# Performance work log

Hardware: AMD Instinct MI355X
Metric: run time of the kernel (lower is better)

Reference implementation:

```python
import jax, jax.numpy as jnp
import numpy as np

B, H, S, D = 1, 16, 2048, 64


def setup_inputs() -> dict:
    key = jax.random.key(0)
    kq, kk, kv, km = jax.random.split(key, 4)
    q = jax.random.normal(kq, (B, H, S, D), dtype=jnp.float32)
    k = jax.random.normal(kk, (B, H, S, D), dtype=jnp.float32)
    v = jax.random.normal(kv, (B, H, S, D), dtype=jnp.float32)
    omask = jax.random.uniform(km, (B, H, S, S), dtype=jnp.float32)
    return {"q": q, "k": k, "v": v, "omask": omask}


def reference(q, k, v, omask):
    # mask = omask / sqrt(rowsum(omask)), nan -> 0
    row_sum = jnp.sum(omask, axis=-1, keepdims=True)  # [B,H,S,1]
    decay_mask = jnp.nan_to_num(omask / jnp.sqrt(row_sum), nan=0.0)
    # retention = (q k^T) * mask  -> [B,H,S,S]
    retention = jnp.einsum("bhsd,bhtd->bhst", q, k) * decay_mask
    # normalize by |rowsum(retention)| clamped to >= 1 (detached in original)
    scale = jnp.clip(jnp.abs(jnp.sum(retention, axis=-1, keepdims=True)), 1.0, None)
    retention = retention / scale
    # output = retention @ v -> [B,H,S,D]
    return jnp.einsum("bhst,bhtd->bhsd", retention, v)
```

## Files before the change

### kernel.cpp

```cpp
#include <hip/hip_runtime.h>

#define H 16
#define S 2048
#define D 64
#define BM 64
#define BN 64
#define NT (S / BN)

typedef __attribute__((ext_vector_type(8))) short bf16x8;
typedef __attribute__((ext_vector_type(4))) short short4v;
typedef __attribute__((ext_vector_type(4))) float fx4;

static __device__ __forceinline__ short f2bf(float x) {
    unsigned u = __float_as_uint(x);
    u += 0x7fffu + ((u >> 16) & 1u);
    return (short)(u >> 16);
}
static __device__ __forceinline__ float bf2f(short s) {
    return __uint_as_float(((unsigned)(unsigned short)s) << 16);
}
static __device__ __forceinline__ void gl_lds16(const void* g, void* l) {
    __builtin_amdgcn_global_load_lds(
        (const __attribute__((address_space(1))) unsigned int*)g,
        (__attribute__((address_space(3))) unsigned int*)l, 16, 0, 0);
}

__global__ __launch_bounds__(256)
void ParallelRetention_prep_kernel(
    const float* __restrict__ k, const float* __restrict__ v,
    short* __restrict__ khi, short* __restrict__ klo, short* __restrict__ vt)
{
    __shared__ short lv[64 * 72];
    const int tid = threadIdx.x;
    const int h  = blockIdx.x & 15;
    const int sb = blockIdx.x >> 4;
    const int s0 = sb * 64;
    const int t_base = (tid >> 4) << 2;
    const int d4     = (tid & 15) << 2;
    const size_t hoff = (size_t)h * S * D;

    {
        const float* kb = k + hoff + (size_t)(s0 + t_base) * D + d4;
#pragma unroll
        for (int r = 0; r < 4; ++r) {
            fx4 kr = *(const fx4*)(kb + (size_t)r * D);
            short4v h4, l4;
#pragma unroll
            for (int j = 0; j < 4; ++j) {
                short hi = f2bf(kr[j]);
                h4[j] = hi;
                l4[j] = f2bf(kr[j] - bf2f(hi));
            }
            *(short4v*)(&khi[hoff + (size_t)(s0 + t_base + r) * D + d4]) = h4;
            *(short4v*)(&klo[hoff + (size_t)(s0 + t_base + r) * D + d4]) = l4;
        }
    }
    {
        const float* vb = v + hoff + (size_t)(s0 + t_base) * D + d4;
        fx4 vr[4];
#pragma unroll
        for (int r = 0; r < 4; ++r) vr[r] = *(const fx4*)(vb + (size_t)r * D);
#pragma unroll
        for (int j = 0; j < 4; ++j) {
            short4v p;
#pragma unroll
            for (int r = 0; r < 4; ++r) p[r] = f2bf(vr[r][j]);
            *(short4v*)(&lv[(d4 + j) * 72 + t_base]) = p;
        }
    }
    __syncthreads();
    {
        const int d = tid >> 2;
        const int c = tid & 3;
        bf16x8 a = *(const bf16x8*)(&lv[d * 72 + c * 16]);
        bf16x8 b = *(const bf16x8*)(&lv[d * 72 + c * 16 + 8]);
        short* o = vt + (size_t)h * D * S + (size_t)d * S + s0 + c * 16;
        *(bf16x8*)(o)     = a;
        *(bf16x8*)(o + 8) = b;
    }
}

__global__ __launch_bounds__(256, 2)
void ParallelRetention_origin_25374666785438_kernel(
    const float* __restrict__ q, const float* __restrict__ om,
    const short* __restrict__ khi, const short* __restrict__ klo,
    const short* __restrict__ vt, float* __restrict__ out)
{
    __shared__ short ldsKh[2][64 * 64];
    __shared__ short ldsKl[2][64 * 64];
    __shared__ short ldsVT[2][64 * 64];
    __shared__ short ldsP[64 * 64];

    const int tid  = threadIdx.x;
    const int wave = tid >> 6;
    const int lane = tid & 63;
    const int col  = lane & 15;
    const int quad = lane >> 4;

    const int h  = blockIdx.x & 15;
    const int qb = blockIdx.x >> 4;
    const int row0 = qb * BM;

    const size_t headQK = (size_t)h * S * D;
    const size_t headM  = (size_t)h * S * S;

    bf16x8 qh[2], qlo[2];
    {
        const int s_row = row0 + wave * 16 + col;
        const float* qp = q + headQK + (size_t)s_row * D + quad * 8;
#pragma unroll
        for (int c = 0; c < 2; ++c) {
            fx4 a = *(const fx4*)(qp + c * 32);
            fx4 b = *(const fx4*)(qp + c * 32 + 4);
            float f[8] = {a[0],a[1],a[2],a[3],b[0],b[1],b[2],b[3]};
#pragma unroll
            for (int j = 0; j < 8; ++j) {
                short hi = f2bf(f[j]);
                qh[c][j]  = hi;
                qlo[c][j] = f2bf(f[j] - bf2f(hi));
            }
        }
    }

    fx4 U[4];
#pragma unroll
    for (int nt = 0; nt < 4; ++nt) { U[nt][0]=0.f; U[nt][1]=0.f; U[nt][2]=0.f; U[nt][3]=0.f; }
    float rs_acc = 0.f, T_acc = 0.f;

    const int xq   = quad ^ (col & 3);
    const int cx   = (col >> 2) & 1;
    const int rdC0 = col * 64 + xq * 8 + cx * 32;
    const int rdC1 = col * 64 + xq * 8 + (cx ^ 1) * 32;
    const int prow   = wave * 16 + col;
    const int pwBase = prow * 64 + (quad & 1) * 4 + (((quad >> 1) ^ (col & 1))) * 8;
    const int pxor   = (col >> 1) & 3;
    const int prC0   = prow * 64 + xq * 8 + cx * 32;
    const int prC1   = prow * 64 + xq * 8 + (cx ^ 1) * 32;
    const int rowl = lane >> 3;
    const int swz8 = ((lane & 7) ^ rowl) * 8;
    const int kSrcOff = rowl * 64 + swz8;
    const int vSrcOff = rowl * 2048 + swz8;

    const short* khiH = khi + headQK;
    const short* kloH = klo + headQK;
    const short* vtH  = vt + (size_t)h * D * S;
    const float* omp0 = om + headM + (size_t)(row0 + wave * 16 + col) * S + quad * 4;

    auto stage = [&](int t0, short* dKh, short* dKl, short* dVT) {
        const short* ks = khiH + (size_t)t0 * 64 + kSrcOff;
        const short* ls = kloH + (size_t)t0 * 64 + kSrcOff;
        const short* vs = vtH + t0 + vSrcOff;
#pragma unroll
        for (int c = 0; c < 6; ++c) {
            int id = wave * 6 + c;
            int j  = id & 7;
            int tile = id >> 3;
            if (tile == 0)      gl_lds16(ks + j * 512, dKh + j * 512);
            else if (tile == 1) gl_lds16(ls + j * 512, dKl + j * 512);
            else                gl_lds16(vs + (size_t)j * 8 * 2048, dVT + j * 512);
        }
    };
    auto load_om = [&](int t0, fx4 (&o)[4]) {
#pragma unroll
        for (int tn = 0; tn < 4; ++tn)
            o[tn] = *(const fx4*)(omp0 + t0 + tn * 16);
    };
    auto compute = [&](const short* Kh, const short* Kl, const short* VT,
                       const fx4 (&omc)[4]) {
#pragma unroll
        for (int tn = 0; tn < 4; ++tn) {
            bf16x8 kh0 = *(const bf16x8*)(&Kh[tn * 1024 + rdC0]);
            bf16x8 kh1 = *(const bf16x8*)(&Kh[tn * 1024 + rdC1]);
            bf16x8 kl0 = *(const bf16x8*)(&Kl[tn * 1024 + rdC0]);
            bf16x8 kl1 = *(const bf16x8*)(&Kl[tn * 1024 + rdC1]);
            fx4 z; z[0]=0.f; z[1]=0.f; z[2]=0.f; z[3]=0.f;
            z = __builtin_amdgcn_mfma_f32_16x16x32_bf16(kh0, qh[0],  z, 0, 0, 0);
            z = __builtin_amdgcn_mfma_f32_16x16x32_bf16(kh1, qh[1],  z, 0, 0, 0);
            z = __builtin_amdgcn_mfma_f32_16x16x32_bf16(kl0, qh[0],  z, 0, 0, 0);
            z = __builtin_amdgcn_mfma_f32_16x16x32_bf16(kl1, qh[1],  z, 0, 0, 0);
            z = __builtin_amdgcn_mfma_f32_16x16x32_bf16(kh0, qlo[0], z, 0, 0, 0);
            z = __builtin_amdgcn_mfma_f32_16x16x32_bf16(kh1, qlo[1], z, 0, 0, 0);
            short4v p4;
#pragma unroll
            for (int r = 0; r < 4; ++r) {
                float m = omc[tn][r];
                float p = z[r] * m;
                rs_acc += m;
                T_acc  += p;
                p4[r] = f2bf(p);
            }
            *(short4v*)(&ldsP[pwBase + ((tn ^ pxor) << 4)]) = p4;
        }
        bf16x8 pa0 = *(const bf16x8*)(&ldsP[prC0]);
        bf16x8 pa1 = *(const bf16x8*)(&ldsP[prC1]);
#pragma unroll
        for (int nt = 0; nt < 4; ++nt) {
            bf16x8 vb0 = *(const bf16x8*)(&VT[nt * 1024 + rdC0]);
            bf16x8 vb1 = *(const bf16x8*)(&VT[nt * 1024 + rdC1]);
            U[nt] = __builtin_amdgcn_mfma_f32_16x16x32_bf16(pa0, vb0, U[nt], 0, 0, 0);
            U[nt] = __builtin_amdgcn_mfma_f32_16x16x32_bf16(pa1, vb1, U[nt], 0, 0, 0);
        }
    };

    fx4 omA[4], omB[4];
    stage(0, &ldsKh[0][0], &ldsKl[0][0], &ldsVT[0][0]);
    load_om(0, omA);

    for (int t = 0; t < NT; t += 2) {
        __syncthreads();
        if (t + 1 < NT) {
            stage((t + 1) * BN, &ldsKh[1][0], &ldsKl[1][0], &ldsVT[1][0]);
            load_om((t + 1) * BN, omB);
        }
        compute(&ldsKh[0][0], &ldsKl[0][0], &ldsVT[0][0], omA);
        __syncthreads();
        if (t + 2 < NT) {
            stage((t + 2) * BN, &ldsKh[0][0], &ldsKl[0][0], &ldsVT[0][0]);
            load_om((t + 2) * BN, omA);
        }
        compute(&ldsKh[1][0], &ldsKl[1][0], &ldsVT[1][0], omB);
    }

    rs_acc += __shfl_xor(rs_acc, 16, 64);
    rs_acc += __shfl_xor(rs_acc, 32, 64);
    T_acc  += __shfl_xor(T_acc, 16, 64);
    T_acc  += __shfl_xor(T_acc, 32, 64);
    float inv = rs_acc > 0.f ? rsqrtf(rs_acc) : 0.f;
    float rowsum = T_acc * inv;
    float sc = fabsf(rowsum);
    sc = sc < 1.f ? 1.f : sc;
    float fac = inv / sc;
    float f[4];
#pragma unroll
    for (int r = 0; r < 4; ++r) f[r] = __shfl(fac, quad * 4 + r, 64);
    float* op = out + headQK + (size_t)(row0 + wave * 16) * D;
#pragma unroll
    for (int r = 0; r < 4; ++r)
#pragma unroll
        for (int nt = 0; nt < 4; ++nt)
            op[(size_t)(quad * 4 + r) * D + nt * 16 + col] = U[nt][r] * f[r];
}

extern "C" void kernel_launch(void* const* d_in, const int* in_sizes, int n_in,
                              void* d_out, int out_size, void* d_ws, size_t ws_size,
                              hipStream_t stream) {
    const float* q  = (const float*)d_in[0];
    const float* k  = (const float*)d_in[1];
    const float* v  = (const float*)d_in[2];
    const float* om = (const float*)d_in[3];
    float* out = (float*)d_out;
    (void)in_sizes; (void)n_in; (void)out_size; (void)ws_size;

    short* khi = (short*)d_ws;
    short* klo = khi + (size_t)H * S * D;
    short* vt  = klo + (size_t)H * S * D;

    hipLaunchKernelGGL(ParallelRetention_prep_kernel,
                       dim3(H * (S / 64)), dim3(256), 0, stream, k, v, khi, klo, vt);
    hipLaunchKernelGGL(ParallelRetention_origin_25374666785438_kernel,
                       dim3(H * (S / BM)), dim3(256), 0, stream, q, om, khi, klo, vt, out);
}
```

Baseline: 394.7 us.

## Switch QK^T to 32x32x16 MFMA and split key tiles across wave pairs

Reorganizes work so each pair of waves owns 32 query rows and each wave in the pair handles half of the 64-key tile. The QK^T product now uses 32x32x16 bf16 MFMAs with hi/lo split accumulators, and each wave keeps a private P buffer in LDS, so the 16x16 MFMAs for P·V contract only that wave's 32 keys. The two halves' partial outputs and row sums are combined at the end through LDS scratch reused from the K buffers. The aim is fewer LDS fragment loads and better MFMA efficiency, at the cost of more registers, a cross-wave reduction with extra syncs, and half the waves idle during the output write.

```diff
diff --git a/kernel.cpp b/kernel.cpp
--- a/kernel.cpp
+++ b/kernel.cpp
@@ -10,6 +10,7 @@
 typedef __attribute__((ext_vector_type(8))) short bf16x8;
 typedef __attribute__((ext_vector_type(4))) short short4v;
 typedef __attribute__((ext_vector_type(4))) float fx4;
+typedef __attribute__((ext_vector_type(16))) float f32x16;
 
 static __device__ __forceinline__ short f2bf(float x) {
     unsigned u = __float_as_uint(x);
@@ -89,13 +90,17 @@
     __shared__ short ldsKh[2][64 * 64];
     __shared__ short ldsKl[2][64 * 64];
     __shared__ short ldsVT[2][64 * 64];
-    __shared__ short ldsP[64 * 64];
+    __shared__ short ldsP[4][32 * 64];
 
     const int tid  = threadIdx.x;
     const int wave = tid >> 6;
     const int lane = tid & 63;
-    const int col  = lane & 15;
-    const int quad = lane >> 4;
+    const int rg   = wave >> 1;
+    const int khd  = wave & 1;
+    const int ql   = lane & 31;
+    const int hi   = lane >> 5;
+    const int col16 = lane & 15;
+    const int quad  = lane >> 4;
 
     const int h  = blockIdx.x & 15;
     const int qb = blockIdx.x >> 4;
@@ -104,38 +109,44 @@
     const size_t headQK = (size_t)h * S * D;
     const size_t headM  = (size_t)h * S * S;
 
-    bf16x8 qh[2], qlo[2];
+    bf16x8 qh[4], qlo[4];
     {
-        const int s_row = row0 + wave * 16 + col;
-        const float* qp = q + headQK + (size_t)s_row * D + quad * 8;
-#pragma unroll
-        for (int c = 0; c < 2; ++c) {
-            fx4 a = *(const fx4*)(qp + c * 32);
-            fx4 b = *(const fx4*)(qp + c * 32 + 4);
+        const float* qp = q + headQK + (size_t)(row0 + rg * 32 + ql) * D + hi * 8;
+#pragma unroll
+        for (int c = 0; c < 4; ++c) {
+            fx4 a = *(const fx4*)(qp + c * 16);
+            fx4 b = *(const fx4*)(qp + c * 16 + 4);
             float f[8] = {a[0],a[1],a[2],a[3],b[0],b[1],b[2],b[3]};
 #pragma unroll
             for (int j = 0; j < 8; ++j) {
-                short hi = f2bf(f[j]);
-                qh[c][j]  = hi;
-                qlo[c][j] = f2bf(f[j] - bf2f(hi));
+                short s = f2bf(f[j]);
+                qh[c][j]  = s;
+                qlo[c][j] = f2bf(f[j] - bf2f(s));
             }
         }
     }
 
-    fx4 U[4];
-#pragma unroll
-    for (int nt = 0; nt < 4; ++nt) { U[nt][0]=0.f; U[nt][1]=0.f; U[nt][2]=0.f; U[nt][3]=0.f; }
+    fx4 U[2][4];
+#pragma unroll
+    for (int qs = 0; qs < 2; ++qs)
+#pragma unroll
+        for (int nt = 0; nt < 4; ++nt) { U[qs][nt][0]=0.f; U[qs][nt][1]=0.f; U[qs][nt][2]=0.f; U[qs][nt][3]=0.f; }
     float rs_acc = 0.f, T_acc = 0.f;
 
-    const int xq   = quad ^ (col & 3);
-    const int cx   = (col >> 2) & 1;
-    const int rdC0 = col * 64 + xq * 8 + cx * 32;
-    const int rdC1 = col * 64 + xq * 8 + (cx ^ 1) * 32;
-    const int prow   = wave * 16 + col;
-    const int pwBase = prow * 64 + (quad & 1) * 4 + (((quad >> 1) ^ (col & 1))) * 8;
-    const int pxor   = (col >> 1) & 3;
-    const int prC0   = prow * 64 + xq * 8 + cx * 32;
-    const int prC1   = prow * 64 + xq * 8 + (cx ^ 1) * 32;
+    const int krow = khd * 32 + ql;
+    int rdK[4];
+#pragma unroll
+    for (int c = 0; c < 4; ++c)
+        rdK[c] = krow * 64 + ((((c << 1) + hi) ^ (ql & 7)) << 3);
+    int vtOff[4];
+#pragma unroll
+    for (int nt = 0; nt < 4; ++nt)
+        vtOff[nt] = (nt * 16 + col16) * 64 + (((khd * 4 + quad) ^ (col16 & 7)) << 3);
+    int prOff[2];
+#pragma unroll
+    for (int qs = 0; qs < 2; ++qs)
+        prOff[qs] = (qs * 16 + col16) * 64 + ((quad ^ (col16 & 7)) << 3);
+
     const int rowl = lane >> 3;
     const int swz8 = ((lane & 7) ^ rowl) * 8;
     const int kSrcOff = rowl * 64 + swz8;
@@ -144,7 +155,7 @@
     const short* khiH = khi + headQK;
     const short* kloH = klo + headQK;
     const short* vtH  = vt + (size_t)h * D * S;
-    const float* omp0 = om + headM + (size_t)(row0 + wave * 16 + col) * S + quad * 4;
+    const float* omp0 = om + headM + (size_t)(row0 + rg * 32 + ql) * S + khd * 32 + hi * 4;
 
     auto stage = [&](int t0, short* dKh, short* dKl, short* dVT) {
         const short* ks = khiH + (size_t)t0 * 64 + kSrcOff;
@@ -162,43 +173,49 @@
     };
     auto load_om = [&](int t0, fx4 (&o)[4]) {
 #pragma unroll
-        for (int tn = 0; tn < 4; ++tn)
-            o[tn] = *(const fx4*)(omp0 + t0 + tn * 16);
+        for (int g = 0; g < 4; ++g)
+            o[g] = *(const fx4*)(omp0 + t0 + g * 8);
     };
     auto compute = [&](const short* Kh, const short* Kl, const short* VT,
                        const fx4 (&omc)[4]) {
-#pragma unroll
-        for (int tn = 0; tn < 4; ++tn) {
-            bf16x8 kh0 = *(const bf16x8*)(&Kh[tn * 1024 + rdC0]);
-            bf16x8 kh1 = *(const bf16x8*)(&Kh[tn * 1024 + rdC1]);
-            bf16x8 kl0 = *(const bf16x8*)(&Kl[tn * 1024 + rdC0]);
-            bf16x8 kl1 = *(const bf16x8*)(&Kl[tn * 1024 + rdC1]);
-            fx4 z; z[0]=0.f; z[1]=0.f; z[2]=0.f; z[3]=0.f;
-            z = __builtin_amdgcn_mfma_f32_16x16x32_bf16(kh0, qh[0],  z, 0, 0, 0);
-            z = __builtin_amdgcn_mfma_f32_16x16x32_bf16(kh1, qh[1],  z, 0, 0, 0);
-            z = __builtin_amdgcn_mfma_f32_16x16x32_bf16(kl0, qh[0],  z, 0, 0, 0);
-            z = __builtin_amdgcn_mfma_f32_16x16x32_bf16(kl1, qh[1],  z, 0, 0, 0);
-            z = __builtin_amdgcn_mfma_f32_16x16x32_bf16(kh0, qlo[0], z, 0, 0, 0);
-            z = __builtin_amdgcn_mfma_f32_16x16x32_bf16(kh1, qlo[1], z, 0, 0, 0);
+        bf16x8 kh[4], kl[4];
+#pragma unroll
+        for (int c = 0; c < 4; ++c) {
+            kh[c] = *(const bf16x8*)(&Kh[rdK[c]]);
+            kl[c] = *(const bf16x8*)(&Kl[rdK[c]]);
+        }
+        f32x16 za, zb;
+#pragma unroll
+        for (int i = 0; i < 16; ++i) { za[i] = 0.f; zb[i] = 0.f; }
+#pragma unroll
+        for (int c = 0; c < 4; ++c) za = __builtin_amdgcn_mfma_f32_32x32x16_bf16(kh[c], qh[c],  za, 0, 0, 0);
+#pragma unroll
+        for (int c = 0; c < 4; ++c) zb = __builtin_amdgcn_mfma_f32_32x32x16_bf16(kl[c], qh[c],  zb, 0, 0, 0);
+#pragma unroll
+        for (int c = 0; c < 4; ++c) zb = __builtin_amdgcn_mfma_f32_32x32x16_bf16(kh[c], qlo[c], zb, 0, 0, 0);
+        short* Pw = &ldsP[wave][0];
+#pragma unroll
+        for (int g = 0; g < 4; ++g) {
             short4v p4;
 #pragma unroll
             for (int r = 0; r < 4; ++r) {
-                float m = omc[tn][r];
-                float p = z[r] * m;
+                float m = omc[g][r];
+                float p = (za[g * 4 + r] + zb[g * 4 + r]) * m;
                 rs_acc += m;
                 T_acc  += p;
                 p4[r] = f2bf(p);
             }
-            *(short4v*)(&ldsP[pwBase + ((tn ^ pxor) << 4)]) = p4;
-        }
-        bf16x8 pa0 = *(const bf16x8*)(&ldsP[prC0]);
-        bf16x8 pa1 = *(const bf16x8*)(&ldsP[prC1]);
-#pragma unroll
-        for (int nt = 0; nt < 4; ++nt) {
-            bf16x8 vb0 = *(const bf16x8*)(&VT[nt * 1024 + rdC0]);
-            bf16x8 vb1 = *(const bf16x8*)(&VT[nt * 1024 + rdC1]);
-            U[nt] = __builtin_amdgcn_mfma_f32_16x16x32_bf16(pa0, vb0, U[nt], 0, 0, 0);
-            U[nt] = __builtin_amdgcn_mfma_f32_16x16x32_bf16(pa1, vb1, U[nt], 0, 0, 0);
+            *(short4v*)(&Pw[ql * 64 + ((g ^ (ql & 7)) << 3) + hi * 4]) = p4;
+        }
+        bf16x8 vb[4];
+#pragma unroll
+        for (int nt = 0; nt < 4; ++nt) vb[nt] = *(const bf16x8*)(&VT[vtOff[nt]]);
+#pragma unroll
+        for (int qs = 0; qs < 2; ++qs) {
+            bf16x8 pa = *(const bf16x8*)(&Pw[prOff[qs]]);
+#pragma unroll
+            for (int nt = 0; nt < 4; ++nt)
+                U[qs][nt] = __builtin_amdgcn_mfma_f32_16x16x32_bf16(pa, vb[nt], U[qs][nt], 0, 0, 0);
         }
     };
 
@@ -221,24 +238,46 @@
         compute(&ldsKh[1][0], &ldsKl[1][0], &ldsVT[1][0], omB);
     }
 
-    rs_acc += __shfl_xor(rs_acc, 16, 64);
     rs_acc += __shfl_xor(rs_acc, 32, 64);
-    T_acc  += __shfl_xor(T_acc, 16, 64);
     T_acc  += __shfl_xor(T_acc, 32, 64);
-    float inv = rs_acc > 0.f ? rsqrtf(rs_acc) : 0.f;
-    float rowsum = T_acc * inv;
-    float sc = fabsf(rowsum);
-    sc = sc < 1.f ? 1.f : sc;
-    float fac = inv / sc;
-    float f[4];
-#pragma unroll
-    for (int r = 0; r < 4; ++r) f[r] = __shfl(fac, quad * 4 + r, 64);
-    float* op = out + headQK + (size_t)(row0 + wave * 16) * D;
-#pragma unroll
-    for (int r = 0; r < 4; ++r)
-#pragma unroll
-        for (int nt = 0; nt < 4; ++nt)
-            op[(size_t)(quad * 4 + r) * D + nt * 16 + col] = U[nt][r] * f[r];
+    __syncthreads();
+    float* scrU = (float*)&ldsKh[0][0];
+    float* scrS = (float*)&ldsKl[0][0];
+    if (khd == 1) {
+#pragma unroll
+        for (int qs = 0; qs < 2; ++qs)
+#pragma unroll
+            for (int nt = 0; nt < 4; ++nt)
+#pragma unroll
+                for (int r = 0; r < 4; ++r)
+                    scrU[rg * 2048 + (qs * 16 + quad * 4 + r) * 64 + nt * 16 + col16] = U[qs][nt][r];
+        if (lane < 32) {
+            scrS[rg * 32 + ql] = rs_acc;
+            scrS[64 + rg * 32 + ql] = T_acc;
+        }
+    }
+    __syncthreads();
+    if (khd == 0) {
+        float rs = rs_acc + scrS[rg * 32 + ql];
+        float Tt = T_acc + scrS[64 + rg * 32 + ql];
+        float inv = rs > 0.f ? rsqrtf(rs) : 0.f;
+        float sc = fabsf(Tt * inv);
+        sc = sc < 1.f ? 1.f : sc;
+        float fac = inv / sc;
+        float* op = out + headQK + (size_t)(row0 + rg * 32) * D;
+#pragma unroll
+        for (int qs = 0; qs < 2; ++qs)
+#pragma unroll
+            for (int r = 0; r < 4; ++r) {
+                float f = __shfl(fac, qs * 16 + quad * 4 + r, 64);
+#pragma unroll
+                for (int nt = 0; nt < 4; ++nt) {
+                    float u = U[qs][nt][r] +
+                        scrU[rg * 2048 + (qs * 16 + quad * 4 + r) * 64 + nt * 16 + col16];
+                    op[(size_t)(qs * 16 + quad * 4 + r) * D + nt * 16 + col16] = u * f;
+                }
+            }
+    }
 }
 
 extern "C" void kernel_launch(void* const* d_in, const int* in_sizes, int n_in,
```

Measured after the change: 398.6 us. Within noise of the previous version (+1.0%).
